# Kernel optimization log

Measured on AMD Instinct MI355X. Metric: run time of the kernel, lower is better.

The kernel has to match this reference:

```python
import jax, jax.numpy as jnp
import numpy as np

NUM_GRAPHS = 256
T, F_IN, F_OUT, D_E = 5, 75, 15, 50   # towers, per-tower in, per-tower out, edge emb dim
N_LAYERS = 4
AVG_DEG_LOG = float(np.log(17.0))     # from deg histogram: all nodes have degree 16 -> mean log(deg+1)=log(17)
BN_EPS = 1e-5
STD_EPS = 1e-5


def _pna_conv(h, src, dst, e_enc, pw, pb, qw, qb, lw, lb):
    """One PNAConv layer (divide_input=False, pre_layers=post_layers=1)."""
    N = h.shape[0]
    x_i, x_j = h[dst], h[src]                      # gather target/source node feats [E, F_IN]
    # pre-NN Linear(3*F_IN -> F_IN) per tower, applied to cat([x_i, x_j, e_enc]); split the weight
    Wi, Wj, We = pw[:, :F_IN], pw[:, F_IN:2 * F_IN], pw[:, 2 * F_IN:]
    m = (jnp.einsum('ef,tfg->etg', x_i, Wi)
         + jnp.einsum('ef,tfg->etg', x_j, Wj)
         + jnp.einsum('ef,tfg->etg', e_enc, We) + pb)   # [E, T, F_IN]
    ones = jnp.ones((m.shape[0],), h.dtype)
    cnt = jax.ops.segment_sum(ones, dst, N)        # in-degree per node
    deg = jnp.maximum(cnt, 1.0)[:, None, None]
    mean = jax.ops.segment_sum(m, dst, N) / deg
    mean2 = jax.ops.segment_sum(m * m, dst, N) / deg
    std = jnp.sqrt(jax.nn.relu(mean2 - mean * mean) + STD_EPS)
    has_edge = (cnt > 0)[:, None, None]
    mn = jnp.where(has_edge, jax.ops.segment_min(m, dst, N), 0.0)
    mx = jnp.where(has_edge, jax.ops.segment_max(m, dst, N), 0.0)
    agg = jnp.concatenate([mean, mn, mx, std], axis=-1)          # [N, T, 4*F_IN]
    amp = (jnp.log(jnp.maximum(cnt, 1.0) + 1.0) / AVG_DEG_LOG)[:, None, None]
    out = jnp.concatenate([agg, agg * amp, agg / amp], axis=-1)  # identity/amplification/attenuation [N,T,12*F_IN]
    post = jnp.einsum('ntf,tfg->ntg', out, qw) + qb              # post-NN Linear(900 -> 15) per tower
    return post.reshape(N, T * F_OUT) @ lw + lb                  # mixing Linear(75 -> 75)


def setup_inputs() -> dict:
    key = jax.random.key(0)
    ks = iter(jax.random.split(key, 64))
    N, E = 16384, 262144
    g = lambda shape, s=0.1: jax.random.normal(next(ks), shape, jnp.float32) * s
    return dict(
        x=jax.random.randint(next(ks), (N,), 0, 21),
        edge_index=jax.random.randint(next(ks), (2, E), 0, N),
        edge_attr=jax.random.randint(next(ks), (E,), 0, 4),
        batch=jnp.sort(jax.random.randint(next(ks), (N,), 0, NUM_GRAPHS)),
        node_emb=g((21, F_IN)),
        edge_emb=g((4, D_E)),
        edge_enc_w=g((N_LAYERS, D_E, F_IN)), edge_enc_b=jnp.zeros((N_LAYERS, F_IN)),
        pre_w=g((N_LAYERS, T, 3 * F_IN, F_IN)), pre_b=jnp.zeros((N_LAYERS, T, F_IN)),
        post_w=g((N_LAYERS, T, 12 * F_IN, F_OUT)), post_b=jnp.zeros((N_LAYERS, T, F_OUT)),
        lin_w=g((N_LAYERS, T * F_OUT, T * F_OUT)), lin_b=jnp.zeros((N_LAYERS, T * F_OUT)),
        bn_gamma=jnp.ones((N_LAYERS, 75)), bn_beta=jnp.zeros((N_LAYERS, 75)),
        mlp_w1=g((75, 50)), mlp_b1=jnp.zeros((50,)),
        mlp_w2=g((50, 25)), mlp_b2=jnp.zeros((25,)),
        mlp_w3=g((25, 1)), mlp_b3=jnp.zeros((1,)),
    )


def reference(x, edge_index, edge_attr, batch, node_emb, edge_emb,
              edge_enc_w, edge_enc_b, pre_w, pre_b, post_w, post_b,
              lin_w, lin_b, bn_gamma, bn_beta,
              mlp_w1, mlp_b1, mlp_w2, mlp_b2, mlp_w3, mlp_b3):
    h = node_emb[x]                    # [N, 75]
    e = edge_emb[edge_attr]            # [E, 50]
    src, dst = edge_index[0], edge_index[1]
    for l in range(N_LAYERS):
        e_enc = e @ edge_enc_w[l] + edge_enc_b[l]   # edge encoder Linear(50->75)
        h = _pna_conv(h, src, dst, e_enc, pre_w[l], pre_b[l],
                      post_w[l], post_b[l], lin_w[l], lin_b[l])
        mu = h.mean(0)
        var = ((h - mu) ** 2).mean(0)               # biased batch-norm variance (training mode)
        h = jax.nn.relu((h - mu) / jnp.sqrt(var + BN_EPS) * bn_gamma[l] + bn_beta[l])
    g = jax.ops.segment_sum(h, batch, NUM_GRAPHS)   # global_add_pool [G, 75]
    g = jax.nn.relu(g @ mlp_w1 + mlp_b1)
    g = jax.nn.relu(g @ mlp_w2 + mlp_b2)
    return g @ mlp_w3 + mlp_b3                      # [G, 1]
```

## Files before the change

kernel.cpp:

```cpp
#include <hip/hip_runtime.h>
#include <math.h>

#define N_NODES 16384
#define N_EDGES 262144
#define TOW 5
#define FI 75
#define FO 15
#define DE 50
#define NL 4
#define NG 256
#define HWP 752
#define AGS 1504
#define PNN 4
#define ENB 4

static __device__ __attribute__((aligned(16))) float g_hA[N_NODES*FI];
static __device__ __attribute__((aligned(16))) float g_hB[N_NODES*FI];
static __device__ __attribute__((aligned(16))) float g_hW[N_NODES*HWP];
static __device__ __attribute__((aligned(16))) float g_ec[NL*4*376];
static __device__ int   g_deg[N_NODES];
static __device__ int   g_rowstart[N_NODES+1];
static __device__ int   g_cursor[N_NODES];
static __device__ int   g_edge[N_EDGES];
static __device__ float g_mu[FI];
static __device__ float g_rsig[FI];
static __device__ float g_pool[NG*FI];

__global__ void k_embed(const int* __restrict__ x, const float* __restrict__ node_emb) {
    int i = blockIdx.x * blockDim.x + threadIdx.x;
    if (i < N_NODES*FI) {
        int n = i / FI, f = i % FI;
        g_hA[i] = node_emb[x[n]*FI + f];
    }
}

__global__ void k_zerodeg() {
    int i = blockIdx.x * blockDim.x + threadIdx.x;
    if (i < N_NODES) g_deg[i] = 0;
}

__global__ void k_hist(const int* __restrict__ dst) {
    int e = blockIdx.x * blockDim.x + threadIdx.x;
    if (e < N_EDGES) atomicAdd(&g_deg[dst[e]], 1);
}

__global__ void k_scan() {
    __shared__ int part[1024];
    int t = threadIdx.x;
    int base = t * 16;
    int loc[16];
    int s = 0;
    #pragma unroll
    for (int i = 0; i < 16; i++) { loc[i] = s; s += g_deg[base + i]; }
    part[t] = s;
    __syncthreads();
    for (int off = 1; off < 1024; off <<= 1) {
        int v = 0;
        if (t >= off) v = part[t - off];
        __syncthreads();
        if (t >= off) part[t] += v;
        __syncthreads();
    }
    int excl = (t == 0) ? 0 : part[t - 1];
    #pragma unroll
    for (int i = 0; i < 16; i++) {
        g_rowstart[base + i] = excl + loc[i];
        g_cursor[base + i]   = excl + loc[i];
    }
    if (t == 1023) g_rowstart[N_NODES] = part[1023];
}

__global__ void k_scatter(const int* __restrict__ src, const int* __restrict__ dst,
                          const int* __restrict__ attr) {
    int e = blockIdx.x * blockDim.x + threadIdx.x;
    if (e < N_EDGES) {
        int d = dst[e];
        int pos = atomicAdd(&g_cursor[d], 1);
        g_edge[pos] = src[e] | (attr[e] << 16);
    }
}

__global__ void k_ec(const float* __restrict__ edge_emb, const float* __restrict__ edge_enc_w,
                     const float* __restrict__ edge_enc_b, const float* __restrict__ pre_w,
                     const float* __restrict__ pre_b) {
    int l = blockIdx.x;
    const float* eew = edge_enc_w + l*DE*FI;
    const float* eeb = edge_enc_b + l*FI;
    const float* pw  = pre_w + l*TOW*3*FI*FI;
    const float* pb  = pre_b + l*TOW*FI;
    __shared__ float e_enc[4*FI];
    int t = threadIdx.x;
    if (t < 4*FI) {
        int a = t / FI, f = t % FI;
        float s = eeb[f];
        for (int d = 0; d < DE; d++) s += edge_emb[a*DE + d] * eew[d*FI + f];
        e_enc[t] = s;
    }
    __syncthreads();
    for (int o = t; o < 4*376; o += blockDim.x) {
        int a = o / 376;
        int r = o % 376;
        float s = 0.f;
        if (r < TOW*FI) {
            int tw = r / FI, g = r % FI;
            s = pb[tw*FI + g];
            const float* W = pw + (tw*(3*FI) + 2*FI)*FI + g;
            for (int f = 0; f < FI; f++) s += e_enc[a*FI + f] * W[f*FI];
        }
        g_ec[l*1504 + o] = s;
    }
}

#define NPB 8
__global__ void k_hw(const float* __restrict__ pw, const float* __restrict__ gamma,
                     const float* __restrict__ beta, int first) {
    __shared__ float hsh[NPB*FI];
    int n0 = blockIdx.x * NPB;
    int tid = threadIdx.x;
    for (int i = tid; i < NPB*FI; i += blockDim.x) {
        int idx = (n0 + i/FI)*FI + (i % FI);
        float v;
        if (first) {
            v = g_hA[idx];
        } else {
            int c = i % FI;
            v = (g_hB[idx] - g_mu[c]) * g_rsig[c] * gamma[c] + beta[c];
            v = v > 0.f ? v : 0.f;
        }
        hsh[i] = v;
    }
    __syncthreads();
    for (int o = tid; o < 2*TOW*FI; o += blockDim.x) {
        int half = o / (TOW*FI);
        int r = o % (TOW*FI);
        int tw = r / FI, g = r % FI;
        const float* W = pw + (tw*(3*FI) + half*FI)*FI + g;
        float acc[NPB];
        #pragma unroll
        for (int nn = 0; nn < NPB; nn++) acc[nn] = 0.f;
        for (int f = 0; f < FI; f++) {
            float w = W[f*FI];
            #pragma unroll
            for (int nn = 0; nn < NPB; nn++) acc[nn] += hsh[nn*FI + f] * w;
        }
        #pragma unroll
        for (int nn = 0; nn < NPB; nn++)
            g_hW[(n0+nn)*HWP + half*376 + r] = acc[nn];
    }
}

__global__ __launch_bounds__(128*ENB) void k_edge(int l, float* __restrict__ agg) {
    int tid = threadIdx.x;
    int wp  = tid >> 7;
    int q   = tid & 127;
    int n   = blockIdx.x * ENB + wp;
    bool act = q < 94;
    const float* ec = g_ec + l*1504;
    int e0 = g_rowstart[n], e1 = g_rowstart[n+1];
    int cnt = e1 - e0;

    float s0=0.f,s1=0.f,s2=0.f,s3=0.f;
    float t0=0.f,t1=0.f,t2=0.f,t3=0.f;
    float mn0=1e30f,mn1=1e30f,mn2=1e30f,mn3=1e30f;
    float mx0=-1e30f,mx1=-1e30f,mx2=-1e30f,mx3=-1e30f;
    float h0=0.f,h1=0.f,h2=0.f,h3=0.f;
    if (act) {
        float4 hv = *(const float4*)&g_hW[n*HWP + 4*q];
        h0=hv.x; h1=hv.y; h2=hv.z; h3=hv.w;
    }

    for (int e = e0; e < e1; e += 4) {
        int i1 = e+1, i2 = e+2, i3 = e+3;
        int pk0 = g_edge[e];
        int pk1 = g_edge[i1 < e1 ? i1 : e];
        int pk2 = g_edge[i2 < e1 ? i2 : e];
        int pk3 = g_edge[i3 < e1 ? i3 : e];
        if (act) {
            float4 hj0 = *(const float4*)&g_hW[(pk0 & 0xFFFF)*HWP + 376 + 4*q];
            float4 hj1 = *(const float4*)&g_hW[(pk1 & 0xFFFF)*HWP + 376 + 4*q];
            float4 hj2 = *(const float4*)&g_hW[(pk2 & 0xFFFF)*HWP + 376 + 4*q];
            float4 hj3 = *(const float4*)&g_hW[(pk3 & 0xFFFF)*HWP + 376 + 4*q];
            float4 ev0 = *(const float4*)&ec[(pk0 >> 16)*376 + 4*q];
            float4 ev1 = *(const float4*)&ec[(pk1 >> 16)*376 + 4*q];
            float4 ev2 = *(const float4*)&ec[(pk2 >> 16)*376 + 4*q];
            float4 ev3 = *(const float4*)&ec[(pk3 >> 16)*376 + 4*q];
            #define ACCUM(ii, hj, ev)                                        \
                if (ii < e1) {                                               \
                    float m0 = h0 + hj.x + ev.x;                             \
                    float m1 = h1 + hj.y + ev.y;                             \
                    float m2 = h2 + hj.z + ev.z;                             \
                    float m3 = h3 + hj.w + ev.w;                             \
                    s0 += m0; s1 += m1; s2 += m2; s3 += m3;                  \
                    t0 += m0*m0; t1 += m1*m1; t2 += m2*m2; t3 += m3*m3;      \
                    mn0 = fminf(mn0,m0); mn1 = fminf(mn1,m1);                \
                    mn2 = fminf(mn2,m2); mn3 = fminf(mn3,m3);                \
                    mx0 = fmaxf(mx0,m0); mx1 = fmaxf(mx1,m1);                \
                    mx2 = fmaxf(mx2,m2); mx3 = fmaxf(mx3,m3);                \
                }
            ACCUM(e,  hj0, ev0)
            ACCUM(i1, hj1, ev1)
            ACCUM(i2, hj2, ev2)
            ACCUM(i3, hj3, ev3)
            #undef ACCUM
        }
    }

    if (act) {
        float inv = 1.0f / ((cnt > 0) ? (float)cnt : 1.0f);
        float sv[4]  = {s0,s1,s2,s3};
        float tv[4]  = {t0,t1,t2,t3};
        float mnv[4] = {mn0,mn1,mn2,mn3};
        float mxv[4] = {mx0,mx1,mx2,mx3};
        float* ar = agg + (size_t)n*AGS;
        #pragma unroll
        for (int j = 0; j < 4; j++) {
            int c = 4*q + j;
            if (c < TOW*FI) {
                int tw = c / FI, f = c - tw*FI;
                float mean  = sv[j]*inv;
                float mean2 = tv[j]*inv;
                float var = mean2 - mean*mean;
                if (var < 0.f) var = 0.f;
                int b = tw*300 + f;
                ar[b      ] = mean;
                ar[b +  75] = (cnt > 0) ? mnv[j] : 0.f;
                ar[b + 150] = (cnt > 0) ? mxv[j] : 0.f;
                ar[b + 225] = sqrtf(var + 1e-5f);
            }
        }
    }
}

__global__ __launch_bounds__(384) void
k_post(const float* __restrict__ agg, const float* __restrict__ qw,
       const float* __restrict__ qb, const float* __restrict__ lw,
       const float* __restrict__ lb) {
    __shared__ __align__(16) float aggs[PNN][AGS];
    __shared__ float part[5*75*5];
    __shared__ float post[PNN][76];
    __shared__ float s_amp[PNN], s_iamp[PNN];
    int tid = threadIdx.x;
    int n0 = blockIdx.x * PNN;

    for (int i = tid; i < PNN*376; i += 384) {
        int nn = i / 376, t4 = i % 376;
        *(float4*)&aggs[nn][4*t4] = *(const float4*)&agg[(size_t)(n0+nn)*AGS + 4*t4];
    }
    if (tid < PNN) {
        int cnt = g_rowstart[n0+tid+1] - g_rowstart[n0+tid];
        float deg = (cnt > 0) ? (float)cnt : 1.0f;
        float amp = logf(deg + 1.0f) * (1.0f/2.8332133440562162f);
        s_amp[tid] = amp; s_iamp[tid] = 1.0f/amp;
    }
    __syncthreads();

    int o = tid % 75, p = tid / 75;
    if (tid < 375) {
        int tw = o / FO, g = o % FO;
        const float* W = qw + tw*900*FO + g;
        float a0[PNN], a1[PNN], a2[PNN];
        #pragma unroll
        for (int nn = 0; nn < PNN; nn++) { a0[nn]=0.f; a1[nn]=0.f; a2[nn]=0.f; }
        int f0 = p*60;
        for (int fq = 0; fq < 15; ++fq) {
            int f = f0 + fq*4;
            float w0a = W[(f  )*FO], w0b = W[(f+1)*FO], w0c = W[(f+2)*FO], w0d = W[(f+3)*FO];
            float w1a = W[(300+f)*FO], w1b = W[(301+f)*FO], w1c = W[(302+f)*FO], w1d = W[(303+f)*FO];
            float w2a = W[(600+f)*FO], w2b = W[(601+f)*FO], w2c = W[(602+f)*FO], w2d = W[(603+f)*FO];
            #pragma unroll
            for (int nn = 0; nn < PNN; nn++) {
                float4 av = *(const float4*)&aggs[nn][tw*300 + f];
                a0[nn] += av.x*w0a + av.y*w0b + av.z*w0c + av.w*w0d;
                a1[nn] += av.x*w1a + av.y*w1b + av.z*w1c + av.w*w1d;
                a2[nn] += av.x*w2a + av.y*w2b + av.z*w2c + av.w*w2d;
            }
        }
        #pragma unroll
        for (int nn = 0; nn < PNN; nn++)
            part[(p*75 + o)*5 + nn] = a0[nn] + s_amp[nn]*a1[nn] + s_iamp[nn]*a2[nn];
    }
    __syncthreads();
    if (tid < 75) {
        #pragma unroll
        for (int nn = 0; nn < PNN; nn++) {
            float s = qb[tid];
            #pragma unroll
            for (int p2 = 0; p2 < 5; p2++) s += part[(p2*75 + tid)*5 + nn];
            post[nn][tid] = s;
        }
    }
    __syncthreads();
    if (tid < 300) {
        int oo = tid % 75, nn = tid / 75;
        const float* Wl = lw + oo;
        float s = lb[oo];
        for (int f = 0; f < 75; f++) s += post[nn][f] * Wl[f*75];
        g_hB[(n0+nn)*FI + oo] = s;
    }
}

__global__ void k_bnstat() {
    int c = blockIdx.x;
    int t = threadIdx.x;
    double s = 0.0, s2 = 0.0;
    for (int n = t; n < N_NODES; n += 256) {
        float v = g_hB[n*FI + c];
        s += v; s2 += (double)v * v;
    }
    __shared__ double ps[256], ps2[256];
    ps[t] = s; ps2[t] = s2;
    __syncthreads();
    for (int off = 128; off > 0; off >>= 1) {
        if (t < off) { ps[t] += ps[t+off]; ps2[t] += ps2[t+off]; }
        __syncthreads();
    }
    if (t == 0) {
        double mu = ps[0] / N_NODES;
        double var = ps2[0] / N_NODES - mu*mu;
        if (var < 0.0) var = 0.0;
        g_mu[c]   = (float)mu;
        g_rsig[c] = (float)(1.0 / sqrt(var + 1e-5));
    }
}

__global__ void k_poolzero() {
    int i = blockIdx.x * blockDim.x + threadIdx.x;
    if (i < NG*FI) g_pool[i] = 0.f;
}

__global__ void k_pool(const int* __restrict__ batch, const float* __restrict__ gamma,
                       const float* __restrict__ beta) {
    int i = blockIdx.x * blockDim.x + threadIdx.x;
    if (i < N_NODES*FI) {
        int n = i / FI, c = i % FI;
        float v = (g_hB[i] - g_mu[c]) * g_rsig[c] * gamma[c] + beta[c];
        v = v > 0.f ? v : 0.f;
        atomicAdd(&g_pool[batch[n]*FI + c], v);
    }
}

__global__ void k_mlp(const float* __restrict__ w1, const float* __restrict__ b1,
                      const float* __restrict__ w2, const float* __restrict__ b2,
                      const float* __restrict__ w3, const float* __restrict__ b3,
                      float* __restrict__ out) {
    __shared__ float gin[FI], h1[50], h2[25];
    int gi = blockIdx.x;
    int t = threadIdx.x;
    if (t < FI) gin[t] = g_pool[gi*FI + t];
    __syncthreads();
    if (t < 50) {
        float s = b1[t];
        for (int f = 0; f < FI; f++) s += gin[f] * w1[f*50 + t];
        h1[t] = s > 0.f ? s : 0.f;
    }
    __syncthreads();
    if (t < 25) {
        float s = b2[t];
        for (int f = 0; f < 50; f++) s += h1[f] * w2[f*25 + t];
        h2[t] = s > 0.f ? s : 0.f;
    }
    __syncthreads();
    if (t == 0) {
        float s = b3[0];
        for (int f = 0; f < 25; f++) s += h2[f] * w3[f];
        out[gi] = s;
    }
}

extern "C" void kernel_launch(void* const* d_in, const int* in_sizes, int n_in,
                              void* d_out, int out_size, void* d_ws, size_t ws_size,
                              hipStream_t stream) {
    const int*   x          = (const int*)  d_in[0];
    const int*   edge_index = (const int*)  d_in[1];
    const int*   edge_attr  = (const int*)  d_in[2];
    const int*   batch      = (const int*)  d_in[3];
    const float* node_emb   = (const float*)d_in[4];
    const float* edge_emb   = (const float*)d_in[5];
    const float* edge_enc_w = (const float*)d_in[6];
    const float* edge_enc_b = (const float*)d_in[7];
    const float* pre_w      = (const float*)d_in[8];
    const float* pre_b      = (const float*)d_in[9];
    const float* post_w     = (const float*)d_in[10];
    const float* post_b     = (const float*)d_in[11];
    const float* lin_w      = (const float*)d_in[12];
    const float* lin_b      = (const float*)d_in[13];
    const float* bn_gamma   = (const float*)d_in[14];
    const float* bn_beta    = (const float*)d_in[15];
    const float* mlp_w1     = (const float*)d_in[16];
    const float* mlp_b1     = (const float*)d_in[17];
    const float* mlp_w2     = (const float*)d_in[18];
    const float* mlp_b2     = (const float*)d_in[19];
    const float* mlp_w3     = (const float*)d_in[20];
    const float* mlp_b3     = (const float*)d_in[21];
    float* out = (float*)d_out;
    float* agg = (float*)d_ws;

    const int* src = edge_index;
    const int* dst = edge_index + N_EDGES;

    k_embed<<<(N_NODES*FI + 255)/256, 256, 0, stream>>>(x, node_emb);
    k_zerodeg<<<(N_NODES + 255)/256, 256, 0, stream>>>();
    k_hist<<<(N_EDGES + 255)/256, 256, 0, stream>>>(dst);
    k_scan<<<1, 1024, 0, stream>>>();
    k_scatter<<<(N_EDGES + 255)/256, 256, 0, stream>>>(src, dst, edge_attr);
    k_ec<<<NL, 512, 0, stream>>>(edge_emb, edge_enc_w, edge_enc_b, pre_w, pre_b);

    for (int l = 0; l < NL; l++) {
        const float* pw  = pre_w  + l*TOW*(3*FI)*FI;
        const float* qw  = post_w + l*TOW*900*FO;
        const float* qb  = post_b + l*TOW*FO;
        const float* lw  = lin_w  + l*(TOW*FO)*(TOW*FO);
        const float* lb  = lin_b  + l*TOW*FO;
        const float* gamP = bn_gamma + (l > 0 ? (l-1)*FI : 0);
        const float* betP = bn_beta  + (l > 0 ? (l-1)*FI : 0);

        k_hw<<<N_NODES/NPB, 256, 0, stream>>>(pw, gamP, betP, l == 0 ? 1 : 0);
        k_edge<<<N_NODES/ENB, 128*ENB, 0, stream>>>(l, agg);
        k_post<<<N_NODES/PNN, 384, 0, stream>>>(agg, qw, qb, lw, lb);
        k_bnstat<<<FI, 256, 0, stream>>>();
    }

    k_poolzero<<<(NG*FI + 255)/256, 256, 0, stream>>>();
    k_pool<<<(N_NODES*FI + 255)/256, 256, 0, stream>>>(batch, bn_gamma + 3*FI, bn_beta + 3*FI);
    k_mlp<<<NG, 128, 0, stream>>>(mlp_w1, mlp_b1, mlp_w2, mlp_b2, mlp_w3, mlp_b3, out);
}
```

Measured before the change: 1.336 ms.

## Transpose aggregation buffer, rewrite post-NN per node-lane, fuse batch-norm stats

The edge kernel now stages its per-node aggregates in shared memory and writes them feature-major (transposed, 4 nodes per float4). A new post kernel maps one node per lane and one tower per wavefront, reading weights uniformly (scalar/broadcast) and coalesced aggregates. BN statistics are accumulated by wave-reduced double atomics inside the post kernel, which removes the separate bnstat launch. The mean and rsig values are recomputed in consumers. The costs are double-precision atomics, a large register footprint (45 accumulators), and the stats being zeroed inside k_edge by block 0.

```diff
diff --git a/kernel.cpp b/kernel.cpp
--- a/kernel.cpp
+++ b/kernel.cpp
@@ -10,21 +10,20 @@
 #define NL 4
 #define NG 256
 #define HWP 752
-#define AGS 1504
-#define PNN 4
+#define ATS 16400
 #define ENB 4
 
 static __device__ __attribute__((aligned(16))) float g_hA[N_NODES*FI];
 static __device__ __attribute__((aligned(16))) float g_hB[N_NODES*FI];
 static __device__ __attribute__((aligned(16))) float g_hW[N_NODES*HWP];
 static __device__ __attribute__((aligned(16))) float g_ec[NL*4*376];
-static __device__ int   g_deg[N_NODES];
-static __device__ int   g_rowstart[N_NODES+1];
-static __device__ int   g_cursor[N_NODES];
-static __device__ int   g_edge[N_EDGES];
-static __device__ float g_mu[FI];
-static __device__ float g_rsig[FI];
-static __device__ float g_pool[NG*FI];
+static __device__ int    g_deg[N_NODES];
+static __device__ int    g_rowstart[N_NODES+1];
+static __device__ int    g_cursor[N_NODES];
+static __device__ int    g_edge[N_EDGES];
+static __device__ double g_bns1[FI];
+static __device__ double g_bns2[FI];
+static __device__ float  g_pool[NG*FI];
 
 __global__ void k_embed(const int* __restrict__ x, const float* __restrict__ node_emb) {
     int i = blockIdx.x * blockDim.x + threadIdx.x;
@@ -124,7 +123,12 @@
             v = g_hA[idx];
         } else {
             int c = i % FI;
-            v = (g_hB[idx] - g_mu[c]) * g_rsig[c] * gamma[c] + beta[c];
+            double mud  = g_bns1[c] * (1.0/N_NODES);
+            double vard = g_bns2[c] * (1.0/N_NODES) - mud*mud;
+            if (vard < 0.0) vard = 0.0;
+            float mu   = (float)mud;
+            float rsig = (float)(1.0 / sqrt(vard + 1e-5));
+            v = (g_hB[idx] - mu) * rsig * gamma[c] + beta[c];
             v = v > 0.f ? v : 0.f;
         }
         hsh[i] = v;
@@ -149,8 +153,10 @@
     }
 }
 
-__global__ __launch_bounds__(128*ENB) void k_edge(int l, float* __restrict__ agg) {
+__global__ __launch_bounds__(128*ENB) void k_edge(int l, float* __restrict__ aggT) {
+    __shared__ float aggl[ENB][1504];
     int tid = threadIdx.x;
+    if (blockIdx.x == 0 && tid < FI) { g_bns1[tid] = 0.0; g_bns2[tid] = 0.0; }
     int wp  = tid >> 7;
     int q   = tid & 127;
     int n   = blockIdx.x * ENB + wp;
@@ -211,7 +217,6 @@
         float tv[4]  = {t0,t1,t2,t3};
         float mnv[4] = {mn0,mn1,mn2,mn3};
         float mxv[4] = {mx0,mx1,mx2,mx3};
-        float* ar = agg + (size_t)n*AGS;
         #pragma unroll
         for (int j = 0; j < 4; j++) {
             int c = 4*q + j;
@@ -222,104 +227,79 @@
                 float var = mean2 - mean*mean;
                 if (var < 0.f) var = 0.f;
                 int b = tw*300 + f;
-                ar[b      ] = mean;
-                ar[b +  75] = (cnt > 0) ? mnv[j] : 0.f;
-                ar[b + 150] = (cnt > 0) ? mxv[j] : 0.f;
-                ar[b + 225] = sqrtf(var + 1e-5f);
+                aggl[wp][b      ] = mean;
+                aggl[wp][b +  75] = (cnt > 0) ? mnv[j] : 0.f;
+                aggl[wp][b + 150] = (cnt > 0) ? mxv[j] : 0.f;
+                aggl[wp][b + 225] = sqrtf(var + 1e-5f);
             }
         }
     }
-}
-
-__global__ __launch_bounds__(384) void
-k_post(const float* __restrict__ agg, const float* __restrict__ qw,
-       const float* __restrict__ qb, const float* __restrict__ lw,
-       const float* __restrict__ lb) {
-    __shared__ __align__(16) float aggs[PNN][AGS];
-    __shared__ float part[5*75*5];
-    __shared__ float post[PNN][76];
-    __shared__ float s_amp[PNN], s_iamp[PNN];
-    int tid = threadIdx.x;
-    int n0 = blockIdx.x * PNN;
-
-    for (int i = tid; i < PNN*376; i += 384) {
-        int nn = i / 376, t4 = i % 376;
-        *(float4*)&aggs[nn][4*t4] = *(const float4*)&agg[(size_t)(n0+nn)*AGS + 4*t4];
-    }
-    if (tid < PNN) {
-        int cnt = g_rowstart[n0+tid+1] - g_rowstart[n0+tid];
-        float deg = (cnt > 0) ? (float)cnt : 1.0f;
-        float amp = logf(deg + 1.0f) * (1.0f/2.8332133440562162f);
-        s_amp[tid] = amp; s_iamp[tid] = 1.0f/amp;
-    }
-    __syncthreads();
-
-    int o = tid % 75, p = tid / 75;
-    if (tid < 375) {
-        int tw = o / FO, g = o % FO;
-        const float* W = qw + tw*900*FO + g;
-        float a0[PNN], a1[PNN], a2[PNN];
-        #pragma unroll
-        for (int nn = 0; nn < PNN; nn++) { a0[nn]=0.f; a1[nn]=0.f; a2[nn]=0.f; }
-        int f0 = p*60;
-        for (int fq = 0; fq < 15; ++fq) {
-            int f = f0 + fq*4;
-            float w0a = W[(f  )*FO], w0b = W[(f+1)*FO], w0c = W[(f+2)*FO], w0d = W[(f+3)*FO];
-            float w1a = W[(300+f)*FO], w1b = W[(301+f)*FO], w1c = W[(302+f)*FO], w1d = W[(303+f)*FO];
-            float w2a = W[(600+f)*FO], w2b = W[(601+f)*FO], w2c = W[(602+f)*FO], w2d = W[(603+f)*FO];
-            #pragma unroll
-            for (int nn = 0; nn < PNN; nn++) {
-                float4 av = *(const float4*)&aggs[nn][tw*300 + f];
-                a0[nn] += av.x*w0a + av.y*w0b + av.z*w0c + av.w*w0d;
-                a1[nn] += av.x*w1a + av.y*w1b + av.z*w1c + av.w*w1d;
-                a2[nn] += av.x*w2a + av.y*w2b + av.z*w2c + av.w*w2d;
-            }
-        }
-        #pragma unroll
-        for (int nn = 0; nn < PNN; nn++)
-            part[(p*75 + o)*5 + nn] = a0[nn] + s_amp[nn]*a1[nn] + s_iamp[nn]*a2[nn];
-    }
-    __syncthreads();
-    if (tid < 75) {
-        #pragma unroll
-        for (int nn = 0; nn < PNN; nn++) {
-            float s = qb[tid];
-            #pragma unroll
-            for (int p2 = 0; p2 < 5; p2++) s += part[(p2*75 + tid)*5 + nn];
-            post[nn][tid] = s;
-        }
-    }
-    __syncthreads();
-    if (tid < 300) {
-        int oo = tid % 75, nn = tid / 75;
-        const float* Wl = lw + oo;
-        float s = lb[oo];
-        for (int f = 0; f < 75; f++) s += post[nn][f] * Wl[f*75];
-        g_hB[(n0+nn)*FI + oo] = s;
-    }
-}
-
-__global__ void k_bnstat() {
-    int c = blockIdx.x;
-    int t = threadIdx.x;
-    double s = 0.0, s2 = 0.0;
-    for (int n = t; n < N_NODES; n += 256) {
-        float v = g_hB[n*FI + c];
-        s += v; s2 += (double)v * v;
-    }
-    __shared__ double ps[256], ps2[256];
-    ps[t] = s; ps2[t] = s2;
-    __syncthreads();
-    for (int off = 128; off > 0; off >>= 1) {
-        if (t < off) { ps[t] += ps[t+off]; ps2[t] += ps2[t+off]; }
-        __syncthreads();
-    }
-    if (t == 0) {
-        double mu = ps[0] / N_NODES;
-        double var = ps2[0] / N_NODES - mu*mu;
-        if (var < 0.0) var = 0.0;
-        g_mu[c]   = (float)mu;
-        g_rsig[c] = (float)(1.0 / sqrt(var + 1e-5));
+    __syncthreads();
+    int n0 = blockIdx.x * ENB;
+    for (int c = tid; c < 1500; c += 128*ENB) {
+        float4 v = make_float4(aggl[0][c], aggl[1][c], aggl[2][c], aggl[3][c]);
+        *(float4*)&aggT[(size_t)c*ATS + n0] = v;
+    }
+}
+
+__global__ __launch_bounds__(320) void
+k_post2(const float* __restrict__ aggT, const float* __restrict__ qw,
+        const float* __restrict__ qb, const float* __restrict__ lw,
+        const float* __restrict__ lb) {
+    __shared__ float postl[FI*64];
+    int lane = threadIdx.x;
+    int tw   = __builtin_amdgcn_readfirstlane(threadIdx.y);
+    int n0 = blockIdx.x * 64;
+    int n  = n0 + lane;
+    int cnt = g_rowstart[n+1] - g_rowstart[n];
+    float deg = (cnt > 0) ? (float)cnt : 1.0f;
+    float amp = logf(deg + 1.0f) * (1.0f/2.8332133440562162f);
+    float iamp = 1.0f/amp;
+
+    const float* A = aggT + (size_t)(tw*300)*ATS + n0;
+    const float* W = qw + tw*13500;
+
+    float a0[15], a1[15], a2[15];
+    #pragma unroll
+    for (int o = 0; o < 15; o++) { a0[o]=0.f; a1[o]=0.f; a2[o]=0.f; }
+    for (int f = 0; f < 300; f += 2) {
+        float av0 = A[(size_t)(f  )*ATS + lane];
+        float av1 = A[(size_t)(f+1)*ATS + lane];
+        #pragma unroll
+        for (int o = 0; o < 15; o++) {
+            a0[o] += av0*W[f*15+o]          + av1*W[(f+1)*15+o];
+            a1[o] += av0*W[4500+f*15+o]     + av1*W[4500+(f+1)*15+o];
+            a2[o] += av0*W[9000+f*15+o]     + av1*W[9000+(f+1)*15+o];
+        }
+    }
+    #pragma unroll
+    for (int o = 0; o < 15; o++)
+        postl[(tw*15+o)*64 + lane] = qb[tw*15+o] + a0[o] + amp*a1[o] + iamp*a2[o];
+    __syncthreads();
+
+    float c0[15];
+    #pragma unroll
+    for (int o = 0; o < 15; o++) c0[o] = 0.f;
+    for (int f = 0; f < FI; f++) {
+        float pv = postl[f*64 + lane];
+        #pragma unroll
+        for (int o = 0; o < 15; o++) c0[o] += pv * lw[f*FI + tw*15 + o];
+    }
+    #pragma unroll
+    for (int o = 0; o < 15; o++) {
+        int c = tw*15 + o;
+        float v = c0[o] + lb[c];
+        g_hB[n*FI + c] = v;
+        float s = v, s2 = v*v;
+        #pragma unroll
+        for (int d = 1; d < 64; d <<= 1) {
+            s  += __shfl_xor(s,  d);
+            s2 += __shfl_xor(s2, d);
+        }
+        if (lane == 0) {
+            atomicAdd(&g_bns1[c], (double)s);
+            atomicAdd(&g_bns2[c], (double)s2);
+        }
     }
 }
 
@@ -333,7 +313,12 @@
     int i = blockIdx.x * blockDim.x + threadIdx.x;
     if (i < N_NODES*FI) {
         int n = i / FI, c = i % FI;
-        float v = (g_hB[i] - g_mu[c]) * g_rsig[c] * gamma[c] + beta[c];
+        double mud  = g_bns1[c] * (1.0/N_NODES);
+        double vard = g_bns2[c] * (1.0/N_NODES) - mud*mud;
+        if (vard < 0.0) vard = 0.0;
+        float mu   = (float)mud;
+        float rsig = (float)(1.0 / sqrt(vard + 1e-5));
+        float v = (g_hB[i] - mu) * rsig * gamma[c] + beta[c];
         v = v > 0.f ? v : 0.f;
         atomicAdd(&g_pool[batch[n]*FI + c], v);
     }
@@ -392,8 +377,8 @@
     const float* mlp_b2     = (const float*)d_in[19];
     const float* mlp_w3     = (const float*)d_in[20];
     const float* mlp_b3     = (const float*)d_in[21];
-    float* out = (float*)d_out;
-    float* agg = (float*)d_ws;
+    float* out  = (float*)d_out;
+    float* aggT = (float*)d_ws;
 
     const int* src = edge_index;
     const int* dst = edge_index + N_EDGES;
@@ -415,9 +400,8 @@
         const float* betP = bn_beta  + (l > 0 ? (l-1)*FI : 0);
 
         k_hw<<<N_NODES/NPB, 256, 0, stream>>>(pw, gamP, betP, l == 0 ? 1 : 0);
-        k_edge<<<N_NODES/ENB, 128*ENB, 0, stream>>>(l, agg);
-        k_post<<<N_NODES/PNN, 384, 0, stream>>>(agg, qw, qb, lw, lb);
-        k_bnstat<<<FI, 256, 0, stream>>>();
+        k_edge<<<N_NODES/ENB, 128*ENB, 0, stream>>>(l, aggT);
+        k_post2<<<dim3(N_NODES/64), dim3(64,5), 0, stream>>>(aggT, qw, qb, lw, lb);
     }
 
     k_poolzero<<<(NG*FI + 255)/256, 256, 0, stream>>>();
```

Result: slower. 1.487 ms (+11.3%).
